# Kernel tuning notes

Measured on AMD Instinct MI355X. Metric: run time of the kernel, lower is better.

## Reference

```python
import jax, jax.numpy as jnp
import numpy as np

C = 1.0          # curvature
TOP_K = 5
LAMBDA_H = 0.01
TAU = 0.1        # forward default
NEG_SAMPLES = 20 # forward default
EPS = 1e-9
B, D = 4096, 64


def _to_ball(v):
    # map gaussian vectors strictly inside the unit Poincare ball
    return 0.8 * v / (1.0 + jnp.linalg.norm(v, axis=-1, keepdims=True))


def setup_inputs() -> dict:
    key = jax.random.key(0)
    ka, kt = jax.random.split(key)
    audio = _to_ball(jax.random.normal(ka, (B, D), dtype=jnp.float32))
    text = _to_ball(jax.random.normal(kt, (B, D), dtype=jnp.float32))
    return {"audio_embeds": audio, "text_embeds": text}


def _pairwise_poincare(x, y, c=C):
    # ||x-y||^2 via gemm instead of materializing [N,N,D] diff tensor
    x_sq = jnp.sum(x * x, axis=-1, keepdims=True)          # [N,1]
    y_sq = jnp.sum(y * y, axis=-1, keepdims=True).T        # [1,M]
    diff_sq = jnp.maximum(x_sq + y_sq - 2.0 * (x @ y.T), 0.0)
    x_cl = jnp.minimum(x_sq, 1.0 - EPS)
    y_cl = jnp.minimum(y_sq, 1.0 - EPS)
    denom = jnp.maximum((1.0 - x_cl) * (1.0 - y_cl), EPS)
    z = jnp.maximum(1.0 + 2.0 * diff_sq / denom, 1.0 + EPS)
    return jnp.arccosh(z) / jnp.sqrt(jnp.asarray(c, x.dtype))


def _topk_triplet(embeds, key):
    n = embeds.shape[0]
    dist = _pairwise_poincare(embeds, embeds)
    dist = dist.at[jnp.arange(n), jnp.arange(n)].set(jnp.inf)  # fill_diagonal_(inf)
    k = min(TOP_K, n - 1)
    neg_pos, pos_idx = jax.lax.top_k(-dist, k)                 # k smallest distances
    pos_term = jax.scipy.special.logsumexp(neg_pos / TAU, axis=1)  # logsumexp(-pos_dist/tau)
    # mask out top-k positives (diagonal stays in pool, holding +inf -> exp(-inf)=0)
    mask = jnp.ones((n, n), bool).at[jnp.arange(n)[:, None], pos_idx].set(False)
    # stable argsort: mask-True columns first, in original column order -> matches dist[i][mask[i]]
    order = jnp.argsort(jnp.where(mask, 0, 1), axis=1)
    pool = jnp.take_along_axis(dist, order[:, : n - k], axis=1)    # [n, n-k]
    samp = jax.random.randint(key, (n, NEG_SAMPLES), 0, n - k)
    neg_vals = jnp.take_along_axis(pool, samp, axis=1)             # [n, NEG_SAMPLES]
    neg_term = jax.scipy.special.logsumexp(-neg_vals / TAU, axis=1)
    return jnp.mean(neg_term - pos_term)  # mean of -(pos_term - neg_term)


def reference(audio_embeds, text_embeds):
    # HyperbolicLayeredLoss.forward returns lambda_h * (text_h + audio_h);
    # the cross-modal loss is computed but NOT added to the returned total in the source.
    key_text = jax.random.key(1)
    key_audio = jax.random.key(2)
    loss_text_h = _topk_triplet(text_embeds, key_text)
    loss_audio_h = _topk_triplet(audio_embeds, key_audio)
    return LAMBDA_H * (loss_text_h + loss_audio_h)
```

## Files before the change

### kernel.cpp

```cpp
#include <hip/hip_runtime.h>
#include <stdint.h>

#define JAX_PARTITIONABLE 1

constexpr int N = 4096;
constexpr int DIM = 64;
constexpr int TOPK = 5;
constexpr int NEGS = 20;
constexpr float TAU_ = 0.1f;
constexpr uint32_t SPAN = 4091u;
constexpr uint32_t MULT = 2309u;

constexpr int CQ = 256;
constexpr int NT = CQ / 16;
constexpr int RPB = 64;
constexpr int YSTRIDE = 136;
constexpr int NQB = 4;
constexpr int CAP = 64;

typedef __attribute__((ext_vector_type(8))) short bf16x8;
typedef __attribute__((ext_vector_type(4))) float f32x4;

__device__ __forceinline__ uint32_t rotl32(uint32_t v, int d) {
  return (v << d) | (v >> (32 - d));
}

__device__ __forceinline__ void threefry(uint32_t k0, uint32_t k1,
                                         uint32_t& x0, uint32_t& x1) {
  const uint32_t k2 = k0 ^ k1 ^ 0x1BD11BDAu;
  x0 += k0; x1 += k1;
#define TF_R(r) { x0 += x1; x1 = rotl32(x1, r); x1 ^= x0; }
  TF_R(13) TF_R(15) TF_R(26) TF_R(6)
  x0 += k1; x1 += k2 + 1u;
  TF_R(17) TF_R(29) TF_R(16) TF_R(24)
  x0 += k2; x1 += k0 + 2u;
  TF_R(13) TF_R(15) TF_R(26) TF_R(6)
  x0 += k0; x1 += k1 + 3u;
  TF_R(17) TF_R(29) TF_R(16) TF_R(24)
  x0 += k1; x1 += k2 + 4u;
  TF_R(13) TF_R(15) TF_R(26) TF_R(6)
  x0 += k2; x1 += k0 + 5u;
#undef TF_R
}

__device__ __forceinline__ uint32_t sample_idx(uint32_t seed, uint32_t f) {
#if JAX_PARTITIONABLE
  uint32_t a0 = 0u, a1 = 0u; threefry(0u, seed, a0, a1);
  uint32_t b0 = 0u, b1 = 1u; threefry(0u, seed, b0, b1);
  uint32_t h0 = 0u, h1 = f;  threefry(a0, a1, h0, h1);
  const uint32_t hi = h0 ^ h1;
  uint32_t l0 = 0u, l1 = f;  threefry(b0, b1, l0, l1);
  const uint32_t lo = l0 ^ l1;
#else
  uint32_t a0 = 0u, a1 = 2u; threefry(0u, seed, a0, a1);
  uint32_t c0 = 1u, c1 = 3u; threefry(0u, seed, c0, c1);
  const uint32_t HALF = (uint32_t)(N * NEGS / 2);
  uint32_t hi, lo;
  if (f < HALF) {
    uint32_t x0 = f, x1 = f + HALF; threefry(a0, c0, x0, x1); hi = x0;
    x0 = f; x1 = f + HALF;          threefry(a1, c1, x0, x1); lo = x0;
  } else {
    uint32_t x0 = f - HALF, x1 = f; threefry(a0, c0, x0, x1); hi = x1;
    x0 = f - HALF; x1 = f;          threefry(a1, c1, x0, x1); lo = x1;
  }
#endif
  return ((hi % SPAN) * MULT + (lo % SPAN)) % SPAN;
}

__device__ __forceinline__ float acosh_dev(float z) {
  return logf(z + sqrtf((z - 1.0f) * (z + 1.0f)));
}

__device__ __forceinline__ uint16_t f2bf(float f) {
  const uint32_t u = __float_as_uint(f);
  return (uint16_t)((u + 0x7FFFu + ((u >> 16) & 1u)) >> 16);
}
__device__ __forceinline__ float bf2f(uint16_t h) {
  return __uint_as_float((uint32_t)h << 16);
}

__global__ __launch_bounds__(64) void k_pre(const float* __restrict__ Xa,
                                            const float* __restrict__ Xt,
                                            uint16_t* __restrict__ Xs,
                                            float* __restrict__ ysq,
                                            float* __restrict__ inv,
                                            uint32_t* __restrict__ cnt) {
  const int m = blockIdx.y;
  const float* __restrict__ X = (m == 0) ? Xt : Xa;
  const int i = blockIdx.x * 64 + threadIdx.x;
  const float* xr = X + (size_t)i * DIM;

  uint32_t hb[DIM / 2], lb[DIM / 2];
  float s = 0.0f;
#pragma unroll
  for (int u = 0; u < DIM / 4; ++u) {
    const float4 v = *(const float4*)(xr + 4 * u);
    s = fmaf(v.x, v.x, s); s = fmaf(v.y, v.y, s);
    s = fmaf(v.z, v.z, s); s = fmaf(v.w, v.w, s);
    const uint16_t h0 = f2bf(v.x), h1 = f2bf(v.y), h2 = f2bf(v.z), h3 = f2bf(v.w);
    const uint16_t l0 = f2bf(v.x - bf2f(h0)), l1 = f2bf(v.y - bf2f(h1));
    const uint16_t l2 = f2bf(v.z - bf2f(h2)), l3 = f2bf(v.w - bf2f(h3));
    hb[2 * u]     = (uint32_t)h0 | ((uint32_t)h1 << 16);
    hb[2 * u + 1] = (uint32_t)h2 | ((uint32_t)h3 << 16);
    lb[2 * u]     = (uint32_t)l0 | ((uint32_t)l1 << 16);
    lb[2 * u + 1] = (uint32_t)l2 | ((uint32_t)l3 << 16);
  }
  uint32_t* dst = (uint32_t*)(Xs + (size_t)(m * N + i) * 128);
#pragma unroll
  for (int w = 0; w < 8; ++w) {
    uint4 qh = { hb[4 * w], hb[4 * w + 1], hb[4 * w + 2], hb[4 * w + 3] };
    ((uint4*)dst)[w] = qh;
  }
#pragma unroll
  for (int w = 0; w < 8; ++w) {
    uint4 ql = { lb[4 * w], lb[4 * w + 1], lb[4 * w + 2], lb[4 * w + 3] };
    ((uint4*)dst)[8 + w] = ql;
  }
  ysq[m * N + i] = s;
  inv[m * N + i] = 1.0f / (1.0f - fminf(s, 1.0f));
  cnt[m * N + i] = 0u;
}

__global__ __launch_bounds__(256) void k_bound(
    const uint16_t* __restrict__ Xs, const float* __restrict__ ysq,
    const float* __restrict__ inv, uint64_t* __restrict__ partial) {
  const int rb = (int)blockIdx.x;
  const int qs = (int)blockIdx.y;
  const int m = (int)blockIdx.z;
  const int qr = rb >> 4;
  const int j0q = (qr * NQB + qs) * CQ;

  const int tid = (int)threadIdx.x;
  const int wid = tid >> 6;
  const int l = tid & 63;
  const int i0w = rb * RPB + wid * 16;
  const int mN = m * N;
  const uint16_t* __restrict__ Xm = Xs + (size_t)m * N * 128;
  const int lc = l & 15;
  const int lk = l >> 4;
  const int lk4 = lk * 4;
  const int lk8 = lk * 8;
  const int sr = tid >> 4;
  const int sc8 = (tid & 15) * 8;

  __shared__ __align__(16) unsigned char smem[4 * 16 * YSTRIDE * 2 + 2048];
  uint16_t* ybuf = (uint16_t*)smem;
  float* sq_s = (float*)(smem + 4 * 16 * YSTRIDE * 2);
  float* iv_s = sq_s + CQ;

  bf16x8 xf[2][2];
#pragma unroll
  for (int c = 0; c < 2; ++c)
#pragma unroll
    for (int h = 0; h < 2; ++h)
      xf[c][h] = *(const bf16x8*)(Xm + (size_t)(i0w + lc) * 128 +
                                  h * 64 + c * 32 + lk8);

  const float xsq_i = ysq[mN + i0w + lc];
  const float inv2_i = 2.0f * inv[mN + i0w + lc];
  const int gi = i0w + lc;

  const uint64_t SENT = ((uint64_t)0x7F800000u << 32) | 0xFFFFFFFFu;
  uint64_t t5[TOPK];
#pragma unroll
  for (int t = 0; t < TOPK; ++t) t5[t] = SENT;
  float z5own = __uint_as_float(0x7F800000u);

  const f32x4 zz = {0.0f, 0.0f, 0.0f, 0.0f};
  const float INF_ = __uint_as_float(0x7F800000u);

  {
    if (tid < 64)
      *(float4*)&sq_s[tid * 4] = *(const float4*)&ysq[mN + j0q + tid * 4];
    else if (tid < 128)
      *(float4*)&iv_s[(tid - 64) * 4] =
          *(const float4*)&inv[mN + j0q + (tid - 64) * 4];
    *(uint4*)(ybuf + sr * YSTRIDE + sc8) =
        *(const uint4*)(Xm + (size_t)(j0q + sr) * 128 + sc8);
    *(uint4*)(ybuf + 16 * YSTRIDE + sr * YSTRIDE + sc8) =
        *(const uint4*)(Xm + (size_t)(j0q + 16 + sr) * 128 + sc8);
    __syncthreads();
  }

#define PROCESS(T, BUF)                                                        \
  {                                                                            \
    const uint16_t* yp = (BUF) + lc * YSTRIDE + lk8;                           \
    const bf16x8 Y0 = *(const bf16x8*)(yp);                                    \
    const bf16x8 Y1 = *(const bf16x8*)(yp + 32);                               \
    const bf16x8 Y2 = *(const bf16x8*)(yp + 64);                               \
    const bf16x8 Y3 = *(const bf16x8*)(yp + 96);                               \
    f32x4 acc;                \
    acc = __builtin_amdgcn_mfma_f32_16x16x32_bf16(Y0, xf[0][0], zz, 0, 0, 0);  \
    acc = __builtin_amdgcn_mfma_f32_16x16x32_bf16(Y1, xf[1][0], acc, 0, 0, 0); \
    acc = __builtin_amdgcn_mfma_f32_16x16x32_bf16(Y2, xf[0][0], acc, 0, 0, 0); \
    acc = __builtin_amdgcn_mfma_f32_16x16x32_bf16(Y3, xf[1][0], acc, 0, 0, 0); \
    acc = __builtin_amdgcn_mfma_f32_16x16x32_bf16(Y0, xf[0][1], acc, 0, 0, 0); \
    acc = __builtin_amdgcn_mfma_f32_16x16x32_bf16(Y1, xf[1][1], acc, 0, 0, 0); \
    const float4 sq4 = *(const float4*)&sq_s[(T) * 16 + lk4];                  \
    const float4 iv4 = *(const float4*)&iv_s[(T) * 16 + lk4];                  \
    const int jb = j0q + (T) * 16;                                             \
    float zt[4];                                                               \
    _Pragma("unroll") for (int p = 0; p < 4; ++p) {                            \
      const float yc = (p == 0) ? sq4.x : (p == 1) ? sq4.y                     \
                      : (p == 2) ? sq4.z : sq4.w;                              \
      const float ic = (p == 0) ? iv4.x : (p == 1) ? iv4.y                     \
                      : (p == 2) ? iv4.z : iv4.w;                              \
      const float diff = fmaxf(xsq_i + yc - 2.0f * acc[p], 0.0f);              \
      zt[p] = fmaf(diff * inv2_i, ic, 1.0f);                                   \
    }                                                                          \
    if (jb == i0w) {                                                           \
      _Pragma("unroll") for (int p = 0; p < 4; ++p)                            \
        if (gi == jb + lk4 + p) zt[p] = INF_;                                  \
    }                                                                          \
    const float zm = fminf(fminf(zt[0], zt[1]), fminf(zt[2], zt[3]));          \
    if (zm <= z5own) {                                                         \
      _Pragma("unroll") for (int p = 0; p < 4; ++p) {                          \
        uint64_t key = ((uint64_t)__float_as_uint(zt[p]) << 32) |              \
                       (uint32_t)(jb + lk4 + p);                               \
        if (key < t5[TOPK - 1]) {                                              \
          _Pragma("unroll") for (int tt = 0; tt < TOPK; ++tt) {                \
            const uint64_t cv = t5[tt];                                        \
            if (key < cv) { t5[tt] = key; key = cv; }                          \
          }                                                                    \
        }                                                                      \
      }                                                                        \
      z5own = __uint_as_float((uint32_t)(t5[TOPK - 1] >> 32));                 \
    }                                                                          \
  }

#pragma unroll 1
  for (int T = 0; T < NT; T += 2) {
    const bool hn = (T + 2 < NT);
    uint4 s2, s3;
    if (hn) {
      s2 = *(const uint4*)(Xm + (size_t)(j0q + (T + 2) * 16 + sr) * 128 + sc8);
      s3 = *(const uint4*)(Xm + (size_t)(j0q + (T + 3) * 16 + sr) * 128 + sc8);
    }
    PROCESS(T, ybuf + (size_t)((T) & 3) * 16 * YSTRIDE)
    PROCESS(T + 1, ybuf + (size_t)((T + 1) & 3) * 16 * YSTRIDE)
    if (hn) {
      *(uint4*)(ybuf + (size_t)((T + 2) & 3) * 16 * YSTRIDE + sr * YSTRIDE + sc8) = s2;
      *(uint4*)(ybuf + (size_t)((T + 3) & 3) * 16 * YSTRIDE + sr * YSTRIDE + sc8) = s3;
    }
    __syncthreads();
  }
#undef PROCESS

  uint64_t* mb = (uint64_t*)smem;
#pragma unroll
  for (int t = 0; t < TOPK; ++t)
    mb[((size_t)(wid * 16) + lc) * 21 + lk * TOPK + t] = t5[t];
  __syncthreads();

  if (l < 16) {
    uint64_t cur[TOPK];
#pragma unroll
    for (int t = 0; t < TOPK; ++t) cur[t] = mb[((size_t)(wid * 16) + l) * 21 + t];
    for (int c = 1; c < 4; ++c) {
      for (int t = 0; t < TOPK; ++t) {
        uint64_t key = mb[((size_t)(wid * 16) + l) * 21 + c * TOPK + t];
        if (key >= cur[TOPK - 1]) break;
#pragma unroll
        for (int u = 0; u < TOPK; ++u) {
          const uint64_t cv = cur[u];
          if (key < cv) { cur[u] = key; key = cv; }
        }
      }
    }
#pragma unroll
    for (int t = 0; t < TOPK; ++t)
      partial[((size_t)(m * NQB + qs) * N + i0w + l) * TOPK + t] = cur[t];
  }
}

__global__ __launch_bounds__(256) void k_scan(
    const uint16_t* __restrict__ Xs, const float* __restrict__ ysq,
    const float* __restrict__ inv, const uint64_t* __restrict__ partial,
    uint32_t* __restrict__ cnt, uint64_t* __restrict__ rowlist) {
  const int rb = (int)blockIdx.x;
  const int s = (int)blockIdx.y;
  const int m = (int)blockIdx.z;
  const int qr = rb >> 4;
  const int gs = (s < qr * NQB) ? s : s + NQB;
  const int j0q = gs * CQ;

  const int tid = (int)threadIdx.x;
  const int wid = tid >> 6;
  const int l = tid & 63;
  const int i0w = rb * RPB + wid * 16;
  const int mN = m * N;
  const uint16_t* __restrict__ Xm = Xs + (size_t)m * N * 128;
  const int lc = l & 15;
  const int lk = l >> 4;
  const int lk4 = lk * 4;
  const int lk8 = lk * 8;
  const int sr = tid >> 4;
  const int sc8 = (tid & 15) * 8;
  const int gi = i0w + lc;

  __shared__ __align__(16) unsigned char smem[4 * 16 * YSTRIDE * 2 + 2048];
  uint16_t* ybuf = (uint16_t*)smem;
  float* sq_s = (float*)(smem + 4 * 16 * YSTRIDE * 2);
  float* iv_s = sq_s + CQ;

  bf16x8 xf[2][2];
#pragma unroll
  for (int c = 0; c < 2; ++c)
#pragma unroll
    for (int h = 0; h < 2; ++h)
      xf[c][h] = *(const bf16x8*)(Xm + (size_t)gi * 128 + h * 64 + c * 32 + lk8);

  const float xsq_i = ysq[mN + gi];
  const float inv2_i = 2.0f * inv[mN + gi];

  uint64_t b5[TOPK];
#pragma unroll
  for (int t = 0; t < TOPK; ++t)
    b5[t] = partial[((size_t)(m * NQB) * N + gi) * TOPK + t];
  for (int q = 1; q < NQB; ++q) {
    for (int t = 0; t < TOPK; ++t) {
      uint64_t key = partial[((size_t)(m * NQB + q) * N + gi) * TOPK + t];
      if (key >= b5[TOPK - 1]) break;
#pragma unroll
      for (int u = 0; u < TOPK; ++u) {
        const uint64_t cv = b5[u];
        if (key < cv) { b5[u] = key; key = cv; }
      }
    }
  }
  const uint64_t bound = b5[TOPK - 1];
  const float bz = __uint_as_float((uint32_t)(bound >> 32));

  const f32x4 zz = {0.0f, 0.0f, 0.0f, 0.0f};

  {
    if (tid < 64)
      *(float4*)&sq_s[tid * 4] = *(const float4*)&ysq[mN + j0q + tid * 4];
    else if (tid < 128)
      *(float4*)&iv_s[(tid - 64) * 4] =
          *(const float4*)&inv[mN + j0q + (tid - 64) * 4];
    *(uint4*)(ybuf + sr * YSTRIDE + sc8) =
        *(const uint4*)(Xm + (size_t)(j0q + sr) * 128 + sc8);
    *(uint4*)(ybuf + 16 * YSTRIDE + sr * YSTRIDE + sc8) =
        *(const uint4*)(Xm + (size_t)(j0q + 16 + sr) * 128 + sc8);
    __syncthreads();
  }

#define PSCAN(T, BUF)                                                          \
  {                                                                            \
    const uint16_t* yp = (BUF) + lc * YSTRIDE + lk8;                           \
    const bf16x8 Y0 = *(const bf16x8*)(yp);                                    \
    const bf16x8 Y1 = *(const bf16x8*)(yp + 32);                               \
    const bf16x8 Y2 = *(const bf16x8*)(yp + 64);                               \
    const bf16x8 Y3 = *(const bf16x8*)(yp + 96);                               \
    f32x4 acc;                        \
    acc = __builtin_amdgcn_mfma_f32_16x16x32_bf16(Y0, xf[0][0], zz, 0, 0, 0);  \
    acc = __builtin_amdgcn_mfma_f32_16x16x32_bf16(Y1, xf[1][0], acc, 0, 0, 0); \
    acc = __builtin_amdgcn_mfma_f32_16x16x32_bf16(Y2, xf[0][0], acc, 0, 0, 0); \
    acc = __builtin_amdgcn_mfma_f32_16x16x32_bf16(Y3, xf[1][0], acc, 0, 0, 0); \
    acc = __builtin_amdgcn_mfma_f32_16x16x32_bf16(Y0, xf[0][1], acc, 0, 0, 0); \
    acc = __builtin_amdgcn_mfma_f32_16x16x32_bf16(Y1, xf[1][1], acc, 0, 0, 0); \
    const float4 sq4 = *(const float4*)&sq_s[(T) * 16 + lk4];                  \
    const float4 iv4 = *(const float4*)&iv_s[(T) * 16 + lk4];                  \
    const int jb = j0q + (T) * 16;                                             \
    float zt[4];                                                               \
    _Pragma("unroll") for (int p = 0; p < 4; ++p) {                            \
      const float yc = (p == 0) ? sq4.x : (p == 1) ? sq4.y                     \
                      : (p == 2) ? sq4.z : sq4.w;                              \
      const float ic = (p == 0) ? iv4.x : (p == 1) ? iv4.y                     \
                      : (p == 2) ? iv4.z : iv4.w;                              \
      const float diff = fmaxf(xsq_i + yc - 2.0f * acc[p], 0.0f);              \
      zt[p] = fmaf(diff * inv2_i, ic, 1.0f);                                   \
    }                                                                          \
    const float zm = fminf(fminf(zt[0], zt[1]), fminf(zt[2], zt[3]));          \
    if (zm <= bz) {                   \
      _Pragma("unroll") for (int p = 0; p < 4; ++p) {                          \
        const uint64_t key = ((uint64_t)__float_as_uint(zt[p]) << 32) |        \
                             (uint32_t)(jb + lk4 + p);                         \
        if (key < bound) {                                                     \
          const uint32_t slot = atomicAdd(&cnt[mN + gi], 1u);                  \
          if (slot < (uint32_t)CAP)                                            \
            rowlist[(size_t)(mN + gi) * CAP + slot] = key;                     \
        }                                                                      \
      }                                                                        \
    }                                                                          \
  }

#pragma unroll 1
  for (int T = 0; T < NT; T += 2) {
    const bool hn = (T + 2 < NT);
    uint4 s2, s3;
    if (hn) {
      s2 = *(const uint4*)(Xm + (size_t)(j0q + (T + 2) * 16 + sr) * 128 + sc8);
      s3 = *(const uint4*)(Xm + (size_t)(j0q + (T + 3) * 16 + sr) * 128 + sc8);
    }
    PSCAN(T, ybuf + (size_t)((T) & 3) * 16 * YSTRIDE)
    PSCAN(T + 1, ybuf + (size_t)((T + 1) & 3) * 16 * YSTRIDE)
    if (hn) {
      *(uint4*)(ybuf + (size_t)((T + 2) & 3) * 16 * YSTRIDE + sr * YSTRIDE + sc8) = s2;
      *(uint4*)(ybuf + (size_t)((T + 3) & 3) * 16 * YSTRIDE + sr * YSTRIDE + sc8) = s3;
    }
    __syncthreads();
  }
#undef PSCAN
}

__global__ __launch_bounds__(64) void k_neg(const float* __restrict__ Xa,
                                            const float* __restrict__ Xt,
                                            const float* __restrict__ ysq,
                                            const float* __restrict__ inv,
                                            const uint64_t* __restrict__ partial,
                                            const uint32_t* __restrict__ cnt,
                                            const uint64_t* __restrict__ rowlist,
                                            float* __restrict__ rowres) {
  const int m = blockIdx.y;
  const int i = blockIdx.x;
  const float* __restrict__ X = (m == 0) ? Xt : Xa;
  const uint32_t seed = (m == 0) ? 1u : 2u;
  const int lane = threadIdx.x;

  __shared__ float4 xi4[DIM / 4];
  __shared__ float posv[TOPK];
  if (lane < DIM / 4) xi4[lane] = ((const float4*)(X + (size_t)i * DIM))[lane];
  __syncthreads();

  uint64_t cur[TOPK];
#pragma unroll
  for (int t = 0; t < TOPK; ++t)
    cur[t] = partial[((size_t)(m * NQB) * N + i) * TOPK + t];
  for (int q = 1; q < NQB; ++q) {
    for (int t = 0; t < TOPK; ++t) {
      uint64_t key = partial[((size_t)(m * NQB + q) * N + i) * TOPK + t];
      if (key >= cur[TOPK - 1]) break;
#pragma unroll
      for (int u = 0; u < TOPK; ++u) {
        const uint64_t cv = cur[u];
        if (key < cv) { cur[u] = key; key = cv; }
      }
    }
  }
  {
    const uint32_t c_ = min(cnt[m * N + i], (uint32_t)CAP);
    for (uint32_t sv = 0; sv < c_; ++sv) {
      uint64_t key = rowlist[(size_t)(m * N + i) * CAP + sv];
      if (key < cur[TOPK - 1]) {
#pragma unroll
        for (int u = 0; u < TOPK; ++u) {
          const uint64_t cv = cur[u];
          if (key < cv) { cur[u] = key; key = cv; }
        }
      }
    }
  }

  const float ysq_i = ysq[m * N + i];
  const float inv_i = inv[m * N + i];

  if (lane >= 32 && lane < 32 + TOPK) {
    const int t = lane - 32;
    const uint32_t c = (uint32_t)(cur[t] & 0xffffffffu);
    const float4* xc = (const float4*)(X + (size_t)c * DIM);
    float dot = 0.0f;
#pragma unroll
    for (int k = 0; k < DIM / 4; ++k) {
      const float4 a = xi4[k];
      const float4 b = xc[k];
      dot = fmaf(a.x, b.x, dot); dot = fmaf(a.y, b.y, dot);
      dot = fmaf(a.z, b.z, dot); dot = fmaf(a.w, b.w, dot);
    }
    const float diff = fmaxf(ysq_i + ysq[m * N + c] - 2.0f * dot, 0.0f);
    const float z = 1.0f + 2.0f * diff * inv_i * inv[m * N + c];
    posv[t] = -acosh_dev(z) / TAU_;
  }

  uint32_t pidx[TOPK];
#pragma unroll
  for (int t = 0; t < TOPK; ++t) pidx[t] = (uint32_t)(cur[t] & 0xffffffffu);

#define CSWAP(a, b)                                                           \
  { const uint32_t mn = pidx[a] < pidx[b] ? pidx[a] : pidx[b];                \
    const uint32_t mx = pidx[a] < pidx[b] ? pidx[b] : pidx[a];                \
    pidx[a] = mn; pidx[b] = mx; }
  CSWAP(0, 1) CSWAP(3, 4) CSWAP(2, 4) CSWAP(2, 3) CSWAP(1, 4)
  CSWAP(0, 3) CSWAP(0, 2) CSWAP(1, 3) CSWAP(1, 2)
#undef CSWAP

  float v = -1e30f;
  if (lane < NEGS) {
    const uint32_t f = (uint32_t)i * (uint32_t)NEGS + (uint32_t)lane;
    uint32_t c = sample_idx(seed, f);
#pragma unroll
    for (int t = 0; t < TOPK; ++t) c += (c >= pidx[t]) ? 1u : 0u;
    if (c != (uint32_t)i) {
      const float4* xc = (const float4*)(X + (size_t)c * DIM);
      float dot = 0.0f;
#pragma unroll
      for (int k = 0; k < DIM / 4; ++k) {
        const float4 a = xi4[k];
        const float4 b = xc[k];
        dot = fmaf(a.x, b.x, dot); dot = fmaf(a.y, b.y, dot);
        dot = fmaf(a.z, b.z, dot); dot = fmaf(a.w, b.w, dot);
      }
      const float diff = fmaxf(ysq_i + ysq[m * N + c] - 2.0f * dot, 0.0f);
      const float z = 1.0f + 2.0f * diff * inv_i * inv[m * N + c];
      v = -acosh_dev(z) / TAU_;
    }
  }

  __syncthreads();

  float vmax = v;
#pragma unroll
  for (int o = 32; o > 0; o >>= 1) vmax = fmaxf(vmax, __shfl_xor(vmax, o, 64));
  float e = expf(v - vmax);
  float ss = e;
#pragma unroll
  for (int o = 32; o > 0; o >>= 1) ss += __shfl_xor(ss, o, 64);

  if (lane == 0) {
    float vm = -1e30f;
#pragma unroll
    for (int t = 0; t < TOPK; ++t) vm = fmaxf(vm, posv[t]);
    float ps = 0.0f;
#pragma unroll
    for (int t = 0; t < TOPK; ++t) ps += expf(posv[t] - vm);
    const float pos = vm + logf(ps);
    rowres[m * N + i] = (vmax + logf(ss)) - pos;
  }
}

__global__ __launch_bounds__(256) void k_reduce(const float* __restrict__ rowres,
                                                float* __restrict__ out) {
  __shared__ double sh[256];
  double s = 0.0;
  for (int idx = threadIdx.x; idx < 2 * N; idx += 256) s += (double)rowres[idx];
  sh[threadIdx.x] = s;
  __syncthreads();
  for (int o = 128; o > 0; o >>= 1) {
    if (threadIdx.x < o) sh[threadIdx.x] += sh[threadIdx.x + o];
    __syncthreads();
  }
  if (threadIdx.x == 0) out[0] = (float)(0.01 * (sh[0] / (double)N));
}

extern "C" void kernel_launch(void* const* d_in, const int* in_sizes, int n_in,
                              void* d_out, int out_size, void* d_ws,
                              size_t ws_size, hipStream_t stream) {
  const float* Xa = (const float*)d_in[0];
  const float* Xt = (const float*)d_in[1];
  float* out = (float*)d_out;

  float* ysq = (float*)d_ws;
  float* inv = ysq + 2 * N;
  uint64_t* partial = (uint64_t*)(inv + 2 * N);
  float* rowres = (float*)(partial + (size_t)2 * NQB * N * TOPK);
  uint32_t* cnt = (uint32_t*)(rowres + 2 * N);
  uint64_t* rowlist = (uint64_t*)(cnt + 2 * N);
  uint16_t* Xs = (uint16_t*)(rowlist + (size_t)2 * N * CAP);

  k_pre<<<dim3(N / 64, 2), 64, 0, stream>>>(Xa, Xt, Xs, ysq, inv, cnt);
  k_bound<<<dim3(N / RPB, NQB, 2), 256, 0, stream>>>(Xs, ysq, inv, partial);
  k_scan<<<dim3(N / RPB, 12, 2), 256, 0, stream>>>(Xs, ysq, inv, partial, cnt,
                                                   rowlist);
  k_neg<<<dim3(N, 2), 64, 0, stream>>>(Xa, Xt, ysq, inv, partial, cnt, rowlist,
                                       rowres);
  k_reduce<<<1, 256, 0, stream>>>(rowres, out);
}
```

Measured before the change: 100.1 us.

## Compute exact per-row top-5 bound over all columns, then rescan full matrix

The bound pass used to compute top-5 keys over only 4 of 16 column slabs per row. It now computes a float-only top-5 over every slab using branchless min/max networks, and a new merge kernel reduces these to an exact 5th-smallest z per row. The scan pass then rescans all 16 slabs with that tight bound, keeps only candidates at or below it, and the negative-sampling kernel builds the top-5 from the candidate list alone. This trades a second full pairwise GEMM pass and an extra launch for fewer candidate atomics, a smaller candidate capacity, and no 64-bit key compares in the bound pass.

```diff
diff --git a/kernel.cpp b/kernel.cpp
--- a/kernel.cpp
+++ b/kernel.cpp
@@ -12,11 +12,11 @@
 constexpr uint32_t MULT = 2309u;
 
 constexpr int CQ = 256;
+constexpr int NSLAB = N / CQ;
 constexpr int NT = CQ / 16;
 constexpr int RPB = 64;
 constexpr int YSTRIDE = 136;
-constexpr int NQB = 4;
-constexpr int CAP = 64;
+constexpr int CAP = 32;
 
 typedef __attribute__((ext_vector_type(8))) short bf16x8;
 typedef __attribute__((ext_vector_type(4))) float f32x4;
@@ -121,14 +121,13 @@
   cnt[m * N + i] = 0u;
 }
 
-__global__ __launch_bounds__(256) void k_bound(
+__global__ __launch_bounds__(256) void k_zb(
     const uint16_t* __restrict__ Xs, const float* __restrict__ ysq,
-    const float* __restrict__ inv, uint64_t* __restrict__ partial) {
+    const float* __restrict__ inv, float* __restrict__ zb5) {
   const int rb = (int)blockIdx.x;
-  const int qs = (int)blockIdx.y;
+  const int qq = (int)blockIdx.y;
   const int m = (int)blockIdx.z;
-  const int qr = rb >> 4;
-  const int j0q = (qr * NQB + qs) * CQ;
+  const int j0q = qq * CQ;
 
   const int tid = (int)threadIdx.x;
   const int wid = tid >> 6;
@@ -142,6 +141,7 @@
   const int lk8 = lk * 8;
   const int sr = tid >> 4;
   const int sc8 = (tid & 15) * 8;
+  const int gi = i0w + lc;
 
   __shared__ __align__(16) unsigned char smem[4 * 16 * YSTRIDE * 2 + 2048];
   uint16_t* ybuf = (uint16_t*)smem;
@@ -153,18 +153,14 @@
   for (int c = 0; c < 2; ++c)
 #pragma unroll
     for (int h = 0; h < 2; ++h)
-      xf[c][h] = *(const bf16x8*)(Xm + (size_t)(i0w + lc) * 128 +
-                                  h * 64 + c * 32 + lk8);
-
-  const float xsq_i = ysq[mN + i0w + lc];
-  const float inv2_i = 2.0f * inv[mN + i0w + lc];
-  const int gi = i0w + lc;
-
-  const uint64_t SENT = ((uint64_t)0x7F800000u << 32) | 0xFFFFFFFFu;
-  uint64_t t5[TOPK];
-#pragma unroll
-  for (int t = 0; t < TOPK; ++t) t5[t] = SENT;
-  float z5own = __uint_as_float(0x7F800000u);
+      xf[c][h] = *(const bf16x8*)(Xm + (size_t)gi * 128 + h * 64 + c * 32 + lk8);
+
+  const float xsq_i = ysq[mN + gi];
+  const float inv2_i = 2.0f * inv[mN + gi];
+
+  float t5f[TOPK];
+#pragma unroll
+  for (int t = 0; t < TOPK; ++t) t5f[t] = __uint_as_float(0x7F800000u);
 
   const f32x4 zz = {0.0f, 0.0f, 0.0f, 0.0f};
   const float INF_ = __uint_as_float(0x7F800000u);
@@ -182,14 +178,14 @@
     __syncthreads();
   }
 
-#define PROCESS(T, BUF)                                                        \
+#define PZB(T, BUF)                                                            \
   {                                                                            \
     const uint16_t* yp = (BUF) + lc * YSTRIDE + lk8;                           \
     const bf16x8 Y0 = *(const bf16x8*)(yp);                                    \
     const bf16x8 Y1 = *(const bf16x8*)(yp + 32);                               \
     const bf16x8 Y2 = *(const bf16x8*)(yp + 64);                               \
     const bf16x8 Y3 = *(const bf16x8*)(yp + 96);                               \
-    f32x4 acc;                \
+    f32x4 acc;               \
     acc = __builtin_amdgcn_mfma_f32_16x16x32_bf16(Y0, xf[0][0], zz, 0, 0, 0);  \
     acc = __builtin_amdgcn_mfma_f32_16x16x32_bf16(Y1, xf[1][0], acc, 0, 0, 0); \
     acc = __builtin_amdgcn_mfma_f32_16x16x32_bf16(Y2, xf[0][0], acc, 0, 0, 0); \
@@ -208,23 +204,17 @@
       const float diff = fmaxf(xsq_i + yc - 2.0f * acc[p], 0.0f);              \
       zt[p] = fmaf(diff * inv2_i, ic, 1.0f);                                   \
     }                                                                          \
-    if (jb == i0w) {                                                           \
+    if (jb == i0w) {                           \
       _Pragma("unroll") for (int p = 0; p < 4; ++p)                            \
         if (gi == jb + lk4 + p) zt[p] = INF_;                                  \
     }                                                                          \
-    const float zm = fminf(fminf(zt[0], zt[1]), fminf(zt[2], zt[3]));          \
-    if (zm <= z5own) {                                                         \
-      _Pragma("unroll") for (int p = 0; p < 4; ++p) {                          \
-        uint64_t key = ((uint64_t)__float_as_uint(zt[p]) << 32) |              \
-                       (uint32_t)(jb + lk4 + p);                               \
-        if (key < t5[TOPK - 1]) {                                              \
-          _Pragma("unroll") for (int tt = 0; tt < TOPK; ++tt) {                \
-            const uint64_t cv = t5[tt];                                        \
-            if (key < cv) { t5[tt] = key; key = cv; }                          \
-          }                                                                    \
-        }                                                                      \
+    _Pragma("unroll") for (int p = 0; p < 4; ++p) {                            \
+      float v = zt[p];              \
+      _Pragma("unroll") for (int t = 0; t < TOPK; ++t) {                       \
+        const float mn = fminf(t5f[t], v);                                     \
+        v = fmaxf(t5f[t], v);                                                  \
+        t5f[t] = mn;                                                           \
       }                                                                        \
-      z5own = __uint_as_float((uint32_t)(t5[TOPK - 1] >> 32));                 \
     }                                                                          \
   }
 
@@ -236,53 +226,76 @@
       s2 = *(const uint4*)(Xm + (size_t)(j0q + (T + 2) * 16 + sr) * 128 + sc8);
       s3 = *(const uint4*)(Xm + (size_t)(j0q + (T + 3) * 16 + sr) * 128 + sc8);
     }
-    PROCESS(T, ybuf + (size_t)((T) & 3) * 16 * YSTRIDE)
-    PROCESS(T + 1, ybuf + (size_t)((T + 1) & 3) * 16 * YSTRIDE)
+    PZB(T, ybuf + (size_t)((T) & 3) * 16 * YSTRIDE)
+    PZB(T + 1, ybuf + (size_t)((T + 1) & 3) * 16 * YSTRIDE)
     if (hn) {
       *(uint4*)(ybuf + (size_t)((T + 2) & 3) * 16 * YSTRIDE + sr * YSTRIDE + sc8) = s2;
       *(uint4*)(ybuf + (size_t)((T + 3) & 3) * 16 * YSTRIDE + sr * YSTRIDE + sc8) = s3;
     }
     __syncthreads();
   }
-#undef PROCESS
-
-  uint64_t* mb = (uint64_t*)smem;
+#undef PZB
+
+  float* mb = (float*)smem;
 #pragma unroll
   for (int t = 0; t < TOPK; ++t)
-    mb[((size_t)(wid * 16) + lc) * 21 + lk * TOPK + t] = t5[t];
+    mb[((size_t)(wid * 16) + lc) * 21 + lk * TOPK + t] = t5f[t];
   __syncthreads();
 
   if (l < 16) {
-    uint64_t cur[TOPK];
+    float cur[TOPK];
 #pragma unroll
     for (int t = 0; t < TOPK; ++t) cur[t] = mb[((size_t)(wid * 16) + l) * 21 + t];
     for (int c = 1; c < 4; ++c) {
       for (int t = 0; t < TOPK; ++t) {
-        uint64_t key = mb[((size_t)(wid * 16) + l) * 21 + c * TOPK + t];
-        if (key >= cur[TOPK - 1]) break;
+        float v = mb[((size_t)(wid * 16) + l) * 21 + c * TOPK + t];
+        if (v >= cur[TOPK - 1]) break;
 #pragma unroll
         for (int u = 0; u < TOPK; ++u) {
-          const uint64_t cv = cur[u];
-          if (key < cv) { cur[u] = key; key = cv; }
+          const float mn = fminf(cur[u], v);
+          v = fmaxf(cur[u], v);
+          cur[u] = mn;
         }
       }
     }
 #pragma unroll
     for (int t = 0; t < TOPK; ++t)
-      partial[((size_t)(m * NQB + qs) * N + i0w + l) * TOPK + t] = cur[t];
-  }
+      zb5[((size_t)(m * NSLAB + qq) * N + i0w + l) * TOPK + t] = cur[t];
+  }
+}
+
+__global__ __launch_bounds__(256) void k_zmerge(const float* __restrict__ zb5,
+                                                float* __restrict__ bound) {
+  const int r = (int)blockIdx.x * 256 + (int)threadIdx.x;
+  const int m = r >> 12;
+  const int row = r & (N - 1);
+  float cur[TOPK];
+#pragma unroll
+  for (int t = 0; t < TOPK; ++t)
+    cur[t] = zb5[((size_t)(m * NSLAB) * N + row) * TOPK + t];
+  for (int s = 1; s < NSLAB; ++s) {
+    for (int t = 0; t < TOPK; ++t) {
+      float v = zb5[((size_t)(m * NSLAB + s) * N + row) * TOPK + t];
+      if (v >= cur[TOPK - 1]) break;
+#pragma unroll
+      for (int u = 0; u < TOPK; ++u) {
+        const float mn = fminf(cur[u], v);
+        v = fmaxf(cur[u], v);
+        cur[u] = mn;
+      }
+    }
+  }
+  bound[r] = cur[TOPK - 1];
 }
 
 __global__ __launch_bounds__(256) void k_scan(
     const uint16_t* __restrict__ Xs, const float* __restrict__ ysq,
-    const float* __restrict__ inv, const uint64_t* __restrict__ partial,
+    const float* __restrict__ inv, const float* __restrict__ bound,
     uint32_t* __restrict__ cnt, uint64_t* __restrict__ rowlist) {
   const int rb = (int)blockIdx.x;
-  const int s = (int)blockIdx.y;
+  const int qq = (int)blockIdx.y;
   const int m = (int)blockIdx.z;
-  const int qr = rb >> 4;
-  const int gs = (s < qr * NQB) ? s : s + NQB;
-  const int j0q = gs * CQ;
+  const int j0q = qq * CQ;
 
   const int tid = (int)threadIdx.x;
   const int wid = tid >> 6;
@@ -312,26 +325,10 @@
 
   const float xsq_i = ysq[mN + gi];
   const float inv2_i = 2.0f * inv[mN + gi];
-
-  uint64_t b5[TOPK];
-#pragma unroll
-  for (int t = 0; t < TOPK; ++t)
-    b5[t] = partial[((size_t)(m * NQB) * N + gi) * TOPK + t];
-  for (int q = 1; q < NQB; ++q) {
-    for (int t = 0; t < TOPK; ++t) {
-      uint64_t key = partial[((size_t)(m * NQB + q) * N + gi) * TOPK + t];
-      if (key >= b5[TOPK - 1]) break;
-#pragma unroll
-      for (int u = 0; u < TOPK; ++u) {
-        const uint64_t cv = b5[u];
-        if (key < cv) { b5[u] = key; key = cv; }
-      }
-    }
-  }
-  const uint64_t bound = b5[TOPK - 1];
-  const float bz = __uint_as_float((uint32_t)(bound >> 32));
+  const float bz = bound[mN + gi];
 
   const f32x4 zz = {0.0f, 0.0f, 0.0f, 0.0f};
+  const float INF_ = __uint_as_float(0x7F800000u);
 
   {
     if (tid < 64)
@@ -372,12 +369,16 @@
       const float diff = fmaxf(xsq_i + yc - 2.0f * acc[p], 0.0f);              \
       zt[p] = fmaf(diff * inv2_i, ic, 1.0f);                                   \
     }                                                                          \
+    if (jb == i0w) {                           \
+      _Pragma("unroll") for (int p = 0; p < 4; ++p)                            \
+        if (gi == jb + lk4 + p) zt[p] = INF_;                                  \
+    }                                                                          \
     const float zm = fminf(fminf(zt[0], zt[1]), fminf(zt[2], zt[3]));          \
-    if (zm <= bz) {                   \
+    if (zm <= bz) {                                                            \
       _Pragma("unroll") for (int p = 0; p < 4; ++p) {                          \
-        const uint64_t key = ((uint64_t)__float_as_uint(zt[p]) << 32) |        \
-                             (uint32_t)(jb + lk4 + p);                         \
-        if (key < bound) {                                                     \
+        if (zt[p] <= bz) {                                                     \
+          const uint64_t key = ((uint64_t)__float_as_uint(zt[p]) << 32) |      \
+                               (uint32_t)(jb + lk4 + p);                       \
           const uint32_t slot = atomicAdd(&cnt[mN + gi], 1u);                  \
           if (slot < (uint32_t)CAP)                                            \
             rowlist[(size_t)(mN + gi) * CAP + slot] = key;                     \
@@ -409,7 +410,6 @@
                                             const float* __restrict__ Xt,
                                             const float* __restrict__ ysq,
                                             const float* __restrict__ inv,
-                                            const uint64_t* __restrict__ partial,
                                             const uint32_t* __restrict__ cnt,
                                             const uint64_t* __restrict__ rowlist,
                                             float* __restrict__ rowres) {
@@ -424,21 +424,10 @@
   if (lane < DIM / 4) xi4[lane] = ((const float4*)(X + (size_t)i * DIM))[lane];
   __syncthreads();
 
+  const uint64_t SENT = ((uint64_t)0x7F800000u << 32) | 0xFFFFFFFFu;
   uint64_t cur[TOPK];
 #pragma unroll
-  for (int t = 0; t < TOPK; ++t)
-    cur[t] = partial[((size_t)(m * NQB) * N + i) * TOPK + t];
-  for (int q = 1; q < NQB; ++q) {
-    for (int t = 0; t < TOPK; ++t) {
-      uint64_t key = partial[((size_t)(m * NQB + q) * N + i) * TOPK + t];
-      if (key >= cur[TOPK - 1]) break;
-#pragma unroll
-      for (int u = 0; u < TOPK; ++u) {
-        const uint64_t cv = cur[u];
-        if (key < cv) { cur[u] = key; key = cv; }
-      }
-    }
-  }
+  for (int t = 0; t < TOPK; ++t) cur[t] = SENT;
   {
     const uint32_t c_ = min(cnt[m * N + i], (uint32_t)CAP);
     for (uint32_t sv = 0; sv < c_; ++sv) {
@@ -552,17 +541,18 @@
 
   float* ysq = (float*)d_ws;
   float* inv = ysq + 2 * N;
-  uint64_t* partial = (uint64_t*)(inv + 2 * N);
-  float* rowres = (float*)(partial + (size_t)2 * NQB * N * TOPK);
+  float* bound = inv + 2 * N;
+  float* rowres = bound + 2 * N;
   uint32_t* cnt = (uint32_t*)(rowres + 2 * N);
-  uint64_t* rowlist = (uint64_t*)(cnt + 2 * N);
+  float* zb5 = (float*)(cnt + 2 * N);
+  uint64_t* rowlist = (uint64_t*)(zb5 + (size_t)2 * NSLAB * N * TOPK);
   uint16_t* Xs = (uint16_t*)(rowlist + (size_t)2 * N * CAP);
 
   k_pre<<<dim3(N / 64, 2), 64, 0, stream>>>(Xa, Xt, Xs, ysq, inv, cnt);
-  k_bound<<<dim3(N / RPB, NQB, 2), 256, 0, stream>>>(Xs, ysq, inv, partial);
-  k_scan<<<dim3(N / RPB, 12, 2), 256, 0, stream>>>(Xs, ysq, inv, partial, cnt,
-                                                   rowlist);
-  k_neg<<<dim3(N, 2), 64, 0, stream>>>(Xa, Xt, ysq, inv, partial, cnt, rowlist,
-                                       rowres);
+  k_zb<<<dim3(N / RPB, NSLAB, 2), 256, 0, stream>>>(Xs, ysq, inv, zb5);
+  k_zmerge<<<(2 * N) / 256, 256, 0, stream>>>(zb5, bound);
+  k_scan<<<dim3(N / RPB, NSLAB, 2), 256, 0, stream>>>(Xs, ysq, inv, bound, cnt,
+                                                      rowlist);
+  k_neg<<<dim3(N, 2), 64, 0, stream>>>(Xa, Xt, ysq, inv, cnt, rowlist, rowres);
   k_reduce<<<1, 256, 0, stream>>>(rowres, out);
 }
```

Result: slower. 103.5 us (+3.5%).
